# Performance work log

Hardware: AMD Instinct MI355X
Metric: run time of the kernel (lower is better)

## Reference

```python
import jax, jax.numpy as jnp
import numpy as np

INPUT_DIM = 1024
OUTPUT_DIM = 1024
DEGREE = 8


def setup_inputs() -> dict:
    key = jax.random.key(0)
    k1, k2 = jax.random.split(key)
    x = jax.random.normal(k1, (8192, INPUT_DIM), dtype=jnp.float32)
    std = 1.0 / (INPUT_DIM * (DEGREE + 1))
    cheby_coeffs = jax.random.normal(k2, (INPUT_DIM, OUTPUT_DIM, DEGREE + 1), dtype=jnp.float32) * std
    return {"x": x, "cheby_coeffs": cheby_coeffs}


def reference(x, cheby_coeffs):
    # x: [B, I]; cheby_coeffs: [I, O, D+1]
    degree = cheby_coeffs.shape[-1] - 1
    t = jnp.clip(jnp.tanh(x), -0.999, 0.999)            # [B, I]
    theta = jnp.arccos(t)[..., None]                     # [B, I, 1]
    arange = jnp.arange(degree + 1, dtype=x.dtype)       # [D+1]
    basis = jnp.cos(theta * arange)                      # [B, I, D+1] Chebyshev T_d(t)
    y = jnp.einsum('bid,iod->bo', basis, cheby_coeffs)   # [B, O]
    return y
```

## Files before the change

kernel.cpp:

```cpp
#include <hip/hip_runtime.h>
#include <stdint.h>

#define B_ROWS 8192
#define I_DIM  1024
#define N_DIM  1024
#define NDEG   9
#define K_DIM  (I_DIM * (NDEG-1))

#define BM 256
#define BN 128
#define BK 64
#define NT (K_DIM / BK)

typedef __attribute__((ext_vector_type(8)))  short short8;
typedef __attribute__((ext_vector_type(16))) float f32x16;

__device__ __forceinline__ unsigned short f2bf(float f) {
  union { float f; uint32_t u; } v; v.f = f;
  uint32_t u = v.u;
  u += 0x7FFFu + ((u >> 16) & 1u);
  return (unsigned short)(u >> 16);
}

__device__ __forceinline__ float bf2f(unsigned short h) {
  union { uint32_t u; float f; } v; v.u = ((uint32_t)h) << 16;
  return v.f;
}

__device__ __forceinline__ uint32_t pk_bf16(float lo, float hi) {
  uint32_t r;
  asm("v_cvt_pk_bf16_f32 %0, %1, %2" : "=v"(r) : "v"(lo), "v"(hi));
  return r;
}

__device__ __forceinline__ float fast_tanh(float x) {
  float e = __expf(2.0f * x);
  return 1.0f - __fdividef(2.0f, e + 1.0f);
}

__device__ __forceinline__ int h2(int r) { return (r >> 2) & 7; }

__global__ __launch_bounds__(256) void repack_kernel(const float* __restrict__ cf,
                                                     unsigned short* __restrict__ Bt,
                                                     float* __restrict__ bias) {
  __shared__ unsigned short L[32][584];
  const int i0  = blockIdx.x * 32;
  const int o0  = blockIdx.y * 64;
  const int tid = threadIdx.x;

  #pragma unroll
  for (int j = 0; j < 18; ++j) {
    const int f4  = j * 256 + tid;
    const int il  = f4 / 144;
    const int odq = f4 % 144;
    const float4 v = *reinterpret_cast<const float4*>(
        cf + ((size_t)(i0 + il) * N_DIM + o0) * NDEG + (size_t)odq * 4);
    ushort4 w;
    w.x = f2bf(v.x); w.y = f2bf(v.y); w.z = f2bf(v.z); w.w = f2bf(v.w);
    *reinterpret_cast<ushort4*>(&L[il][odq * 4]) = w;
  }
  __syncthreads();

  const int o  = tid >> 2;
  const int ci = tid & 3;
  const size_t base = (size_t)(o0 + o) * K_DIM + (size_t)(i0 + ci * 8) * 8;
  #pragma unroll
  for (int p = 0; p < 8; ++p) {
    const int il = ci * 8 + p;
    uint4 u;
    u.x = (uint32_t)L[il][o*9 + 1] | ((uint32_t)L[il][o*9 + 2] << 16);
    u.y = (uint32_t)L[il][o*9 + 3] | ((uint32_t)L[il][o*9 + 4] << 16);
    u.z = (uint32_t)L[il][o*9 + 5] | ((uint32_t)L[il][o*9 + 6] << 16);
    u.w = (uint32_t)L[il][o*9 + 7] | ((uint32_t)L[il][o*9 + 8] << 16);
    *reinterpret_cast<uint4*>(Bt + base + (size_t)p * 8) = u;
  }
  if (tid < 64) {
    float s = 0.f;
    #pragma unroll
    for (int il = 0; il < 32; ++il) s += bf2f(L[il][tid * 9]);
    atomicAdd(&bias[o0 + tid], s);
  }
}

__global__ __launch_bounds__(512, 2) void gemm_kernel(const float* __restrict__ x,
                                                      const unsigned short* __restrict__ Bt,
                                                      const float* __restrict__ bias,
                                                      float* __restrict__ C) {
  extern __shared__ unsigned short sm[];
  const int tid  = threadIdx.x;
  const int lane = tid & 63;
  const int wave = tid >> 6;
  const int l31  = lane & 31;
  const int half = lane >> 5;
  const int wm   = wave >> 1;
  const int wn   = wave & 1;

  const int bid = blockIdx.x;
  const int mt  = (bid & 7) + 8 * (bid >> 6);
  const int nt  = (bid >> 3) & 7;
  const int m0  = mt * BM;
  const int n0  = nt * BN;

  const int sr   = tid >> 3;
  const int slot = tid & 7;

  const unsigned short* Bbase = Bt + (size_t)n0 * K_DIM;

  int awoff[4];
  const float* xptr[4];
  #pragma unroll
  for (int q = 0; q < 4; ++q) {
    const int r_ = q * 64 + sr;
    awoff[q] = r_ * 64 + (slot ^ h2(r_)) * 8;
    xptr[q]  = x + (size_t)(m0 + r_) * I_DIM + slot;
  }

  f32x16 acc[2][2];
  #pragma unroll
  for (int a = 0; a < 2; ++a)
    #pragma unroll
    for (int b = 0; b < 2; ++b)
      #pragma unroll
      for (int r = 0; r < 16; ++r)
        acc[a][b][r] = 0.f;

#define STAGE_B2(bf, kk) {                                                                  \
    _Pragma("unroll")                                                                       \
    for (int s_ = 0; s_ < 2; ++s_) {                                                        \
      const int r_ = s_ * 64 + sr; const int gc_ = slot ^ h2(r_);                           \
      __builtin_amdgcn_global_load_lds(                                                     \
        (const __attribute__((address_space(1))) void*)(Bbase + (size_t)r_*K_DIM + (kk) + gc_*8), \
        (__attribute__((address_space(3))) void*)&sm[49152 + (bf)*8192 + r_*64 + slot*8], 16, 0, 0); \
    } }

#define LOADX(xr, tt) {                                                                     \
    _Pragma("unroll")                                                                       \
    for (int q = 0; q < 4; ++q) xr[q] = xptr[q][(tt) * 8]; }

#define BASIS_Q(bf, q, xv) {                                                                \
      float t = fast_tanh(xv);                                                              \
      t = fminf(fmaxf(t, -0.999f), 0.999f);                                                 \
      const float t2 = t + t;                                                               \
      const float T1 = t;                                                                   \
      const float T2 = t2*t - 1.0f;                                                         \
      const float T3 = t2*T2 - T1;                                                          \
      const float T4 = t2*T3 - T2;                                                          \
      const float T5 = t2*T4 - T3;                                                          \
      const float T6 = t2*T5 - T4;                                                          \
      const float T7 = t2*T6 - T5;                                                          \
      const float T8 = t2*T7 - T6;                                                          \
      uint4 u;                                                                              \
      u.x = pk_bf16(T1, T2); u.y = pk_bf16(T3, T4);                                         \
      u.z = pk_bf16(T5, T6); u.w = pk_bf16(T7, T8);                                         \
      *reinterpret_cast<uint4*>(&sm[(bf)*16384 + awoff[q]]) = u; }

  const int rowA0 = wm * 64 + l31;
  const int rowA1 = wm * 64 + 32 + l31;
  const int rowB0 = wn * 64 + l31;
  const int rowB1 = wn * 64 + 32 + l31;
  const int hA0 = h2(rowA0), hA1 = h2(rowA1), hB0 = h2(rowB0), hB1 = h2(rowB1);

#define READ4(Ar, Br, av, bv, ks) {                                                          \
    const int c_ = (ks) * 2 + half;                                                          \
    av[0][ks] = *reinterpret_cast<const short8*>(&(Ar)[rowA0 * 64 + (c_ ^ hA0) * 8]);        \
    av[1][ks] = *reinterpret_cast<const short8*>(&(Ar)[rowA1 * 64 + (c_ ^ hA1) * 8]);        \
    bv[0][ks] = *reinterpret_cast<const short8*>(&(Br)[rowB0 * 64 + (c_ ^ hB0) * 8]);        \
    bv[1][ks] = *reinterpret_cast<const short8*>(&(Br)[rowB1 * 64 + (c_ ^ hB1) * 8]); }

#define MFMA4(av, bv, ks)                                                                    \
    acc[0][0] = __builtin_amdgcn_mfma_f32_32x32x16_bf16(av[0][ks], bv[0][ks], acc[0][0], 0, 0, 0); \
    acc[0][1] = __builtin_amdgcn_mfma_f32_32x32x16_bf16(av[0][ks], bv[1][ks], acc[0][1], 0, 0, 0); \
    acc[1][0] = __builtin_amdgcn_mfma_f32_32x32x16_bf16(av[1][ks], bv[0][ks], acc[1][0], 0, 0, 0); \
    acc[1][1] = __builtin_amdgcn_mfma_f32_32x32x16_bf16(av[1][ks], bv[1][ks], acc[1][1], 0, 0, 0);

#define KS_STEP(AVc, BVc, AVr, BVr, XC, c2_, Ar_, Br_, ks, DO_RD, DO_PREP)                   \
    if (DO_RD) { READ4(Ar_, Br_, AVr, BVr, ks) }                                            \
    if (DO_PREP) { BASIS_Q((c2_), ks, (XC)[ks]) }                                           \
    MFMA4(AVc, BVc, ks)                                                                      \
    if (DO_RD)   __builtin_amdgcn_sched_group_barrier(0x100, 4, 0);                          \
    if (DO_PREP) __builtin_amdgcn_sched_group_barrier(0x200, 1, 0);                          \
    __builtin_amdgcn_sched_group_barrier(0x008, 4, 0);

#define TILE(kt_, AVc, BVc, AVr, BVr, XC, XL, c1_, c2_, DO_RD, DO_PREP, DO_LX, DO_BAR) {     \
    if (DO_PREP) { STAGE_B2((c2_), ((kt_) + 2) * BK) }                                       \
    __builtin_amdgcn_sched_barrier(0);                                                       \
    const unsigned short* Ar_ = &sm[(c1_) * 16384];                                          \
    const unsigned short* Br_ = &sm[49152 + (c1_) * 8192];                                   \
    KS_STEP(AVc, BVc, AVr, BVr, XC, c2_, Ar_, Br_, 0, DO_RD, DO_PREP)                        \
    KS_STEP(AVc, BVc, AVr, BVr, XC, c2_, Ar_, Br_, 1, DO_RD, DO_PREP)                        \
    KS_STEP(AVc, BVc, AVr, BVr, XC, c2_, Ar_, Br_, 2, DO_RD, DO_PREP)                        \
    KS_STEP(AVc, BVc, AVr, BVr, XC, c2_, Ar_, Br_, 3, DO_RD, DO_PREP)                        \
    __builtin_amdgcn_sched_barrier(0);                                                       \
    if (DO_LX) { LOADX(XL, (kt_) + 4) }                                                      \
    if (DO_BAR) {                                                                            \
      if (DO_LX) { asm volatile("s_waitcnt vmcnt(4) lgkmcnt(0)" ::: "memory"); }             \
      else       { asm volatile("s_waitcnt vmcnt(0) lgkmcnt(0)" ::: "memory"); }             \
      __builtin_amdgcn_s_barrier();                                                          \
      __builtin_amdgcn_sched_barrier(0);                                                     \
    } }

  float xrA[4], xrB[4];
  short8 avA[2][4], bvA[2][4], avB[2][4], bvB[2][4];
  LOADX(xrA, 0)
  LOADX(xrB, 1)
  STAGE_B2(0, 0)
  STAGE_B2(1, BK)
  asm volatile("s_waitcnt vmcnt(8)" ::: "memory");
  BASIS_Q(0, 0, xrA[0]) BASIS_Q(0, 1, xrA[1]) BASIS_Q(0, 2, xrA[2]) BASIS_Q(0, 3, xrA[3])
  LOADX(xrA, 2)
  asm volatile("s_waitcnt vmcnt(8)" ::: "memory");
  BASIS_Q(1, 0, xrB[0]) BASIS_Q(1, 1, xrB[1]) BASIS_Q(1, 2, xrB[2]) BASIS_Q(1, 3, xrB[3])
  LOADX(xrB, 3)
  asm volatile("s_waitcnt vmcnt(8) lgkmcnt(0)" ::: "memory");
  __builtin_amdgcn_s_barrier();
  {
    const unsigned short* Ar_ = &sm[0];
    const unsigned short* Br_ = &sm[49152];
    READ4(Ar_, Br_, avA, bvA, 0) READ4(Ar_, Br_, avA, bvA, 1)
    READ4(Ar_, Br_, avA, bvA, 2) READ4(Ar_, Br_, avA, bvA, 3)
  }

  int r0 = 0, r1 = 1, r2 = 2;
  for (int kt = 0; kt < 124; kt += 2) {
    TILE(kt,     avA, bvA, avB, bvB, xrA, xrA, r1, r2, 1, 1, 1, 1)
    TILE(kt + 1, avB, bvB, avA, bvA, xrB, xrB, r2, r0, 1, 1, 1, 1)
    const int t_ = r0; r0 = r2; r2 = r1; r1 = t_;
  }
  TILE(124, avA, bvA, avB, bvB, xrA, xrA, 2, 0, 1, 1, 0, 1)
  TILE(125, avB, bvB, avA, bvA, xrB, xrB, 0, 1, 1, 1, 0, 1)
  TILE(126, avA, bvA, avB, bvB, xrA, xrA, 1, 2, 1, 0, 0, 1)
  TILE(127, avB, bvB, avA, bvA, xrB, xrB, 2, 0, 0, 0, 0, 0)
#undef TILE
#undef KS_STEP
#undef MFMA4
#undef READ4
#undef BASIS_Q
#undef LOADX
#undef STAGE_B2

  #pragma unroll
  for (int ni = 0; ni < 2; ++ni) {
    const int col  = n0 + wn * 64 + ni * 32 + l31;
    const float bc = bias[col];
    #pragma unroll
    for (int mi = 0; mi < 2; ++mi) {
      const int rbase = m0 + wm * 64 + mi * 32 + 4 * half;
      #pragma unroll
      for (int r = 0; r < 16; ++r) {
        const int row = rbase + (r & 3) + 8 * (r >> 2);
        C[(size_t)row * N_DIM + col] = acc[mi][ni][r] + bc;
      }
    }
  }
}

extern "C" void kernel_launch(void* const* d_in, const int* in_sizes, int n_in,
                              void* d_out, int out_size, void* d_ws, size_t ws_size,
                              hipStream_t stream) {
  const float* x      = (const float*)d_in[0];
  const float* coeffs = (const float*)d_in[1];
  float* y            = (float*)d_out;

  const size_t bt_bytes = (size_t)N_DIM * K_DIM * sizeof(unsigned short);
  unsigned short* Bt = (unsigned short*)d_ws;
  float* bias        = (float*)((char*)d_ws + bt_bytes);

  hipMemsetAsync(bias, 0, N_DIM * sizeof(float), stream);

  hipFuncSetAttribute((const void*)gemm_kernel,
                      hipFuncAttributeMaxDynamicSharedMemorySize, 147456);

  repack_kernel<<<dim3(I_DIM / 32, N_DIM / 64), 256, 0, stream>>>(coeffs, Bt, bias);
  gemm_kernel<<<(B_ROWS / BM) * (N_DIM / BN), 512, 147456, stream>>>(x, Bt, bias, y);
}
```

Before: 274.9 us.

## Use one register fragment set with half-tile lookahead LDS reads

Replaces the double-buffered A/B register fragment sets (avA/avB) with a single set. Each tile now reads its remaining two k-slices from the current LDS buffer while issuing MFMAs, then prefetches the first two k-slices of the next buffer. The main loop is unrolled by six so that buffer indices are compile-time constants, and the final tile is peeled. The goal is to cut VGPR pressure and the loop's index-rotation overhead, at the cost of a shorter LDS-to-MFMA lookahead distance.

```diff
diff --git a/kernel.cpp b/kernel.cpp
--- a/kernel.cpp
+++ b/kernel.cpp
@@ -160,78 +160,98 @@
   const int rowB1 = wn * 64 + 32 + l31;
   const int hA0 = h2(rowA0), hA1 = h2(rowA1), hB0 = h2(rowB0), hB1 = h2(rowB1);
 
-#define READ4(Ar, Br, av, bv, ks) {                                                          \
+  short8 av[2][4], bv[2][4];
+
+#define READ4(Ar, Br, ks) {                                                                  \
     const int c_ = (ks) * 2 + half;                                                          \
     av[0][ks] = *reinterpret_cast<const short8*>(&(Ar)[rowA0 * 64 + (c_ ^ hA0) * 8]);        \
     av[1][ks] = *reinterpret_cast<const short8*>(&(Ar)[rowA1 * 64 + (c_ ^ hA1) * 8]);        \
     bv[0][ks] = *reinterpret_cast<const short8*>(&(Br)[rowB0 * 64 + (c_ ^ hB0) * 8]);        \
     bv[1][ks] = *reinterpret_cast<const short8*>(&(Br)[rowB1 * 64 + (c_ ^ hB1) * 8]); }
 
-#define MFMA4(av, bv, ks)                                                                    \
+#define MFMA4(ks)                                                                            \
     acc[0][0] = __builtin_amdgcn_mfma_f32_32x32x16_bf16(av[0][ks], bv[0][ks], acc[0][0], 0, 0, 0); \
     acc[0][1] = __builtin_amdgcn_mfma_f32_32x32x16_bf16(av[0][ks], bv[1][ks], acc[0][1], 0, 0, 0); \
     acc[1][0] = __builtin_amdgcn_mfma_f32_32x32x16_bf16(av[1][ks], bv[0][ks], acc[1][0], 0, 0, 0); \
     acc[1][1] = __builtin_amdgcn_mfma_f32_32x32x16_bf16(av[1][ks], bv[1][ks], acc[1][1], 0, 0, 0);
 
-#define KS_STEP(AVc, BVc, AVr, BVr, XC, c2_, Ar_, Br_, ks, DO_RD, DO_PREP)                   \
-    if (DO_RD) { READ4(Ar_, Br_, AVr, BVr, ks) }                                            \
-    if (DO_PREP) { BASIS_Q((c2_), ks, (XC)[ks]) }                                           \
-    MFMA4(AVc, BVc, ks)                                                                      \
-    if (DO_RD)   __builtin_amdgcn_sched_group_barrier(0x100, 4, 0);                          \
-    if (DO_PREP) __builtin_amdgcn_sched_group_barrier(0x200, 1, 0);                          \
-    __builtin_amdgcn_sched_group_barrier(0x008, 4, 0);
-
-#define TILE(kt_, AVc, BVc, AVr, BVr, XC, XL, c1_, c2_, DO_RD, DO_PREP, DO_LX, DO_BAR) {     \
-    if (DO_PREP) { STAGE_B2((c2_), ((kt_) + 2) * BK) }                                       \
+#define PINS(PREP) \
+    __builtin_amdgcn_sched_group_barrier(0x100, 4, 0);                                       \
+    if (PREP) __builtin_amdgcn_sched_group_barrier(0x200, 1, 0);                             \
+    __builtin_amdgcn_sched_group_barrier(0x008, 4, 0);
+
+#define TILE(kk, c0, c1, c2, XC, PREP, LX, BARV) {                                           \
+    if (PREP) { STAGE_B2(c2, ((kk) + 2) * BK) }                                              \
     __builtin_amdgcn_sched_barrier(0);                                                       \
-    const unsigned short* Ar_ = &sm[(c1_) * 16384];                                          \
-    const unsigned short* Br_ = &sm[49152 + (c1_) * 8192];                                   \
-    KS_STEP(AVc, BVc, AVr, BVr, XC, c2_, Ar_, Br_, 0, DO_RD, DO_PREP)                        \
-    KS_STEP(AVc, BVc, AVr, BVr, XC, c2_, Ar_, Br_, 1, DO_RD, DO_PREP)                        \
-    KS_STEP(AVc, BVc, AVr, BVr, XC, c2_, Ar_, Br_, 2, DO_RD, DO_PREP)                        \
-    KS_STEP(AVc, BVc, AVr, BVr, XC, c2_, Ar_, Br_, 3, DO_RD, DO_PREP)                        \
+    const unsigned short* Ac_ = &sm[(c0) * 16384];                                           \
+    const unsigned short* Bc_ = &sm[49152 + (c0) * 8192];                                    \
+    const unsigned short* An_ = &sm[(c1) * 16384];                                           \
+    const unsigned short* Bn_ = &sm[49152 + (c1) * 8192];                                    \
+    READ4(Ac_, Bc_, 2) if (PREP) { BASIS_Q(c2, 0, (XC)[0]) } MFMA4(0)                        \
+    PINS(PREP)                                                                               \
+    READ4(Ac_, Bc_, 3) if (PREP) { BASIS_Q(c2, 1, (XC)[1]) } MFMA4(1)                        \
+    PINS(PREP)                                                                               \
+    READ4(An_, Bn_, 0) if (PREP) { BASIS_Q(c2, 2, (XC)[2]) } MFMA4(2)                        \
+    PINS(PREP)                                                                               \
+    READ4(An_, Bn_, 1) if (PREP) { BASIS_Q(c2, 3, (XC)[3]) } MFMA4(3)                        \
+    PINS(PREP)                                                                               \
     __builtin_amdgcn_sched_barrier(0);                                                       \
-    if (DO_LX) { LOADX(XL, (kt_) + 4) }                                                      \
-    if (DO_BAR) {                                                                            \
-      if (DO_LX) { asm volatile("s_waitcnt vmcnt(4) lgkmcnt(0)" ::: "memory"); }             \
-      else       { asm volatile("s_waitcnt vmcnt(0) lgkmcnt(0)" ::: "memory"); }             \
-      __builtin_amdgcn_s_barrier();                                                          \
-      __builtin_amdgcn_sched_barrier(0);                                                     \
-    } }
-
-  float xrA[4], xrB[4];
-  short8 avA[2][4], bvA[2][4], avB[2][4], bvB[2][4];
-  LOADX(xrA, 0)
-  LOADX(xrB, 1)
+    if (LX) { LOADX(XC, (kk) + 4) }                                                          \
+    __builtin_amdgcn_sched_barrier(0);                                                       \
+    asm volatile("s_waitcnt vmcnt(" #BARV ") lgkmcnt(0)" ::: "memory");                      \
+    __builtin_amdgcn_s_barrier();                                                            \
+    __builtin_amdgcn_sched_barrier(0); }
+
+  float xrE[4], xrO[4];
+  LOADX(xrE, 0)
+  LOADX(xrO, 1)
   STAGE_B2(0, 0)
   STAGE_B2(1, BK)
   asm volatile("s_waitcnt vmcnt(8)" ::: "memory");
-  BASIS_Q(0, 0, xrA[0]) BASIS_Q(0, 1, xrA[1]) BASIS_Q(0, 2, xrA[2]) BASIS_Q(0, 3, xrA[3])
-  LOADX(xrA, 2)
+  BASIS_Q(0, 0, xrE[0]) BASIS_Q(0, 1, xrE[1]) BASIS_Q(0, 2, xrE[2]) BASIS_Q(0, 3, xrE[3])
+  LOADX(xrE, 2)
   asm volatile("s_waitcnt vmcnt(8)" ::: "memory");
-  BASIS_Q(1, 0, xrB[0]) BASIS_Q(1, 1, xrB[1]) BASIS_Q(1, 2, xrB[2]) BASIS_Q(1, 3, xrB[3])
-  LOADX(xrB, 3)
+  BASIS_Q(1, 0, xrO[0]) BASIS_Q(1, 1, xrO[1]) BASIS_Q(1, 2, xrO[2]) BASIS_Q(1, 3, xrO[3])
+  LOADX(xrO, 3)
   asm volatile("s_waitcnt vmcnt(8) lgkmcnt(0)" ::: "memory");
   __builtin_amdgcn_s_barrier();
   {
     const unsigned short* Ar_ = &sm[0];
     const unsigned short* Br_ = &sm[49152];
-    READ4(Ar_, Br_, avA, bvA, 0) READ4(Ar_, Br_, avA, bvA, 1)
-    READ4(Ar_, Br_, avA, bvA, 2) READ4(Ar_, Br_, avA, bvA, 3)
-  }
-
-  int r0 = 0, r1 = 1, r2 = 2;
-  for (int kt = 0; kt < 124; kt += 2) {
-    TILE(kt,     avA, bvA, avB, bvB, xrA, xrA, r1, r2, 1, 1, 1, 1)
-    TILE(kt + 1, avB, bvB, avA, bvA, xrB, xrB, r2, r0, 1, 1, 1, 1)
-    const int t_ = r0; r0 = r2; r2 = r1; r1 = t_;
-  }
-  TILE(124, avA, bvA, avB, bvB, xrA, xrA, 2, 0, 1, 1, 0, 1)
-  TILE(125, avB, bvB, avA, bvA, xrB, xrB, 0, 1, 1, 1, 0, 1)
-  TILE(126, avA, bvA, avB, bvB, xrA, xrA, 1, 2, 1, 0, 0, 1)
-  TILE(127, avB, bvB, avA, bvA, xrB, xrB, 2, 0, 0, 0, 0, 0)
+    READ4(Ar_, Br_, 0) READ4(Ar_, Br_, 1)
+  }
+
+  for (int kt = 0; kt < 120; kt += 6) {
+    TILE(kt + 0, 0, 1, 2, xrE, 1, 1, 4)
+    TILE(kt + 1, 1, 2, 0, xrO, 1, 1, 4)
+    TILE(kt + 2, 2, 0, 1, xrE, 1, 1, 4)
+    TILE(kt + 3, 0, 1, 2, xrO, 1, 1, 4)
+    TILE(kt + 4, 1, 2, 0, xrE, 1, 1, 4)
+    TILE(kt + 5, 2, 0, 1, xrO, 1, 1, 4)
+  }
+  TILE(120, 0, 1, 2, xrE, 1, 1, 4)
+  TILE(121, 1, 2, 0, xrO, 1, 1, 4)
+  TILE(122, 2, 0, 1, xrE, 1, 1, 4)
+  TILE(123, 0, 1, 2, xrO, 1, 1, 4)
+  TILE(124, 1, 2, 0, xrE, 1, 0, 0)
+  TILE(125, 2, 0, 1, xrO, 1, 0, 0)
+  TILE(126, 0, 1, 2, xrE, 0, 0, 0)
+  {
+    const unsigned short* Ac_ = &sm[16384];
+    const unsigned short* Bc_ = &sm[49152 + 8192];
+    READ4(Ac_, Bc_, 2) MFMA4(0)
+    __builtin_amdgcn_sched_group_barrier(0x100, 4, 0);
+    __builtin_amdgcn_sched_group_barrier(0x008, 4, 0);
+    READ4(Ac_, Bc_, 3) MFMA4(1)
+    __builtin_amdgcn_sched_group_barrier(0x100, 4, 0);
+    __builtin_amdgcn_sched_group_barrier(0x008, 4, 0);
+    MFMA4(2)
+    __builtin_amdgcn_sched_group_barrier(0x008, 4, 0);
+    MFMA4(3)
+    __builtin_amdgcn_sched_group_barrier(0x008, 4, 0);
+  }
 #undef TILE
-#undef KS_STEP
+#undef PINS
 #undef MFMA4
 #undef READ4
 #undef BASIS_Q
```

Result: faster. 262.9 us (-4.4%).
